# Kernel optimization log

Measured on AMD Instinct MI355X. Metric: run time of the kernel, lower is better.

Reference implementation:

```python
import jax, jax.numpy as jnp
import numpy as np

N = 20000      # nodes
E = 320000     # edges (avg degree 16)
F_IN = 32      # raw node feature dim
D = 128        # GNN_EMBEDDING_DIM = out_channels per head
HEADS = 4
RNN_H = 128    # RNN_HIDDEN_DIM
NEG_SLOPE = 0.2


def setup_inputs() -> dict:
    key = jax.random.key(0)
    ks = jax.random.split(key, 16)
    s = 0.05
    return {
        "node_features": jax.random.normal(ks[0], (N, F_IN), jnp.float32),
        "hidden_state": jax.random.normal(ks[1], (1, RNN_H), jnp.float32),
        "W_enc": jax.random.normal(ks[2], (F_IN, D), jnp.float32) * s,
        "b_enc": jax.random.normal(ks[3], (D,), jnp.float32) * s,
        "W_l": jax.random.normal(ks[4], (D, HEADS * D), jnp.float32) * s,
        "b_l": jax.random.normal(ks[5], (HEADS * D,), jnp.float32) * s,
        "W_r": jax.random.normal(ks[6], (D, HEADS * D), jnp.float32) * s,
        "b_r": jax.random.normal(ks[7], (HEADS * D,), jnp.float32) * s,
        "att": jax.random.normal(ks[8], (HEADS, D), jnp.float32) * s,
        "gat_bias": jax.random.normal(ks[9], (D,), jnp.float32) * s,
        "W_ih": jax.random.normal(ks[10], (3 * RNN_H, D), jnp.float32) * s,
        "W_hh": jax.random.normal(ks[11], (3 * RNN_H, RNN_H), jnp.float32) * s,
        "b_ih": jax.random.normal(ks[12], (3 * RNN_H,), jnp.float32) * s,
        "b_hh": jax.random.normal(ks[13], (3 * RNN_H,), jnp.float32) * s,
        "edge_index": jax.random.randint(ks[14], (2, E), 0, N, jnp.int32),
    }


def reference(node_features, hidden_state, W_enc, b_enc, W_l, b_l, W_r, b_r,
              att, gat_bias, W_ih, W_hh, b_ih, b_hh, edge_index):
    n = node_features.shape[0]
    # node encoder + ReLU
    h = jax.nn.relu(node_features @ W_enc + b_enc)                 # [N, D]

    # GATv2Conv (heads=4, concat=False), add_self_loops=True, eval (no dropout)
    loop = jnp.arange(n, dtype=edge_index.dtype)
    src = jnp.concatenate([edge_index[0], loop])                   # source j
    dst = jnp.concatenate([edge_index[1], loop])                   # target i

    xl = (h @ W_l + b_l).reshape(n, HEADS, D)                      # source proj
    xr = (h @ W_r + b_r).reshape(n, HEADS, D)                      # target proj

    e = jax.nn.leaky_relu(xl[src] + xr[dst], NEG_SLOPE)            # [Et, H, C]
    logits = jnp.einsum('ehc,hc->eh', e, att)                      # [Et, H]

    # segment softmax over incoming edges of each target node
    m = jax.ops.segment_max(logits, dst, num_segments=n)           # [N, H]
    m = jnp.where(jnp.isfinite(m), m, 0.0)
    p = jnp.exp(logits - m[dst])
    denom = jax.ops.segment_sum(p, dst, num_segments=n)
    alpha = p / jnp.maximum(denom[dst], 1e-16)                     # [Et, H]

    out = jax.ops.segment_sum(xl[src] * alpha[..., None], dst, num_segments=n)
    gat = out.mean(axis=1) + gat_bias                              # [N, D]

    # agent node 0 -> GRUCell (torch gate order: r, z, n)
    x = gat[0:1]                                                   # [1, D]
    gi = x @ W_ih.T + b_ih
    gh = hidden_state @ W_hh.T + b_hh
    i_r, i_z, i_n = jnp.split(gi, 3, axis=-1)
    h_r, h_z, h_n = jnp.split(gh, 3, axis=-1)
    r = jax.nn.sigmoid(i_r + h_r)
    z = jax.nn.sigmoid(i_z + h_z)
    ng = jnp.tanh(i_n + r * h_n)
    return (1.0 - z) * ng + z * hidden_state                       # [1, RNN_H]
```

## Files before the change

kernel.cpp:

```cpp
#include <hip/hip_runtime.h>


#define NW   32
#define NS   96
#define NBLK (NW + NS)
#define SLOTS 8
#define CAP  40
#define FLAGMAGIC 0x5A5A0000u

#define WEo  0
#define WLo  4096
#define WRo  6144
#define HSo  8192
#define XLo  0
#define LGLo 20480
#define ALPo 21760
#define WIo  21920
#define WHo  23456
#define BUFSZ 24992

#define A_H0  0
#define A_XR  128
#define A_XRP 144
#define A_HP  208
#define A_GH  336
#define A_GIB 348
#define A_GAT 360
#define A_LGP 488
#define A_NF0 528
#define A_BI  560
#define A_BHH 572
#define AUXSZ 584

struct KP {
    const int* ei; int E;
    const float *nf, *W_enc, *b_enc, *W_l, *b_l, *W_r, *b_r, *att, *gat_bias,
                *hprev, *W_ih, *W_hh, *b_ih, *b_hh;
    unsigned *scnt;
    unsigned *xlflag;
    float *hsslot;
    float *lgpart;
    float *xlpub;
    float *out;
};

__device__ __forceinline__ unsigned pollFlag(unsigned* p) {
    for (long it = 0; it < 20000000L; ++it) {
        unsigned v = atomicOr(p, 0u);
        if ((v & 0xFFFF0000u) == FLAGMAGIC) return v & 0xFFFFu;
    }
    return 0u;
}

__device__ __forceinline__ float sigm(float x) { return 1.f / (1.f + expf(-x)); }

__global__ __launch_bounds__(256) void k_all(KP p)
{
    __shared__ __align__(16) float buf[BUFSZ];
    __shared__ __align__(16) float aux[AUXSZ];
    __shared__ int iaux[208];
    const int t = threadIdx.x, b = blockIdx.x;

    if (b >= NW) {
        int s = b - NW;
        if (t == 0) iaux[0] = 0;
        __syncthreads();
        if ((p.E & 3) == 0) {
            int nv = p.E >> 2;
            int per = (nv + NS - 1) / NS;
            int lo = s * per, hi = min(lo + per, nv);
            const int4* d4 = (const int4*)(p.ei + p.E);
            for (int base = lo; base < hi; base += 1024) {
                int4 v[4];
                #pragma unroll
                for (int k = 0; k < 4; ++k) {
                    int i = base + t + k * 256;
                    v[k] = (i < hi) ? d4[i] : make_int4(1, 1, 1, 1);
                }
                #pragma unroll
                for (int k = 0; k < 4; ++k) {
                    int i = base + t + k * 256;
                    if (v[k].x == 0 || v[k].y == 0 || v[k].z == 0 || v[k].w == 0) {
                        #pragma unroll
                        for (int c = 0; c < 4; ++c) {
                            if ((&v[k].x)[c] == 0) {
                                int q = atomicAdd(&iaux[0], 1);
                                if (q < SLOTS) iaux[8 + q] = p.ei[4 * (long)i + c];
                            }
                        }
                    }
                }
            }
        } else {
            int per = (p.E + NS - 1) / NS;
            long lo = (long)s * per, hi = lo + per; if (hi > p.E) hi = p.E;
            for (long i = lo + t; i < hi; i += 256) {
                if (p.ei[p.E + i] == 0) {
                    int q = atomicAdd(&iaux[0], 1);
                    if (q < SLOTS) iaux[8 + q] = p.ei[i];
                }
            }
        }
        for (int idx = t; idx < 1024; idx += 256)
            ((float4*)(buf + WEo))[idx] = ((const float4*)p.W_enc)[idx];
        float bev = (t < 128) ? p.b_enc[t] : 0.f;
        __syncthreads();
        int myc = min(iaux[0], SLOTS);
        if (myc > 0) {
            for (int idx = t; idx < myc * 8; idx += 256) {
                int e = idx >> 3, f4 = idx & 7;
                ((float4*)aux)[e * 8 + f4] =
                    *(const float4*)(p.nf + (long)iaux[8 + e] * 32 + f4 * 4);
            }
            __syncthreads();
            for (int e = 0; e < myc; ++e) {
                if (t < 128) {
                    const float* x = aux + e * 32;
                    float a0 = 0, a1 = 0, a2 = 0, a3 = 0;
                    #pragma unroll
                    for (int k = 0; k < 32; k += 4) {
                        a0 += x[k]     * buf[WEo + k * 128 + t];
                        a1 += x[k + 1] * buf[WEo + (k + 1) * 128 + t];
                        a2 += x[k + 2] * buf[WEo + (k + 2) * 128 + t];
                        a3 += x[k + 3] * buf[WEo + (k + 3) * 128 + t];
                    }
                    p.hsslot[(long)(s * SLOTS + e) * 128 + t] =
                        fmaxf(a0 + a1 + a2 + a3 + bev, 0.f);
                }
            }
        }
        __syncthreads();
        __threadfence();
        if (t == 0) atomicExch(&p.scnt[s * 16], FLAGMAGIC | (unsigned)myc);
        return;
    }

    const int l4 = t & 15, g16 = t >> 4;
    const int j = b * 16 + l4;

    float blv = p.b_l[j], atv = p.att[j];
    float bev = (t < 128) ? p.b_enc[t] : 0.f;
    float brv = (t < 16) ? p.b_r[b * 16 + t] : 0.f;
    if (t < 128) { aux[A_HP + t] = p.hprev[t]; aux[A_GAT + t] = p.gat_bias[t]; }
    if (t >= 128 && t < 140) {
        int rr = t - 128;
        int grow = (rr >> 2) * 128 + b * 4 + (rr & 3);
        aux[A_BI + rr] = p.b_ih[grow];
        aux[A_BHH + rr] = p.b_hh[grow];
    }
    if (t >= 192 && t < 224) aux[A_NF0 + (t - 192)] = p.nf[t - 192];

    for (int idx = t; idx < 1024; idx += 256)
        ((float4*)(buf + WEo))[idx] = ((const float4*)p.W_enc)[idx];
    for (int idx = t; idx < 512; idx += 256) {
        int row = idx >> 2, f4 = idx & 3;
        ((float4*)(buf + WLo))[idx] = *(const float4*)(p.W_l + (long)row * 512 + b * 16 + f4 * 4);
        ((float4*)(buf + WRo))[idx] = *(const float4*)(p.W_r + (long)row * 512 + b * 16 + f4 * 4);
    }
    for (int idx = t; idx < 384; idx += 256) {
        int rr = idx >> 5, f4 = idx & 31;
        int grow = (rr >> 2) * 128 + b * 4 + (rr & 3);
        ((float4*)(buf + WIo))[idx] = *(const float4*)(p.W_ih + (long)grow * 128 + f4 * 4);
        ((float4*)(buf + WHo))[idx] = *(const float4*)(p.W_hh + (long)grow * 128 + f4 * 4);
    }
    __syncthreads();

    if (t < 128) {
        float a0 = 0, a1 = 0, a2 = 0, a3 = 0;
        #pragma unroll
        for (int k = 0; k < 32; k += 4) {
            a0 += aux[A_NF0 + k]     * buf[WEo + k * 128 + t];
            a1 += aux[A_NF0 + k + 1] * buf[WEo + (k + 1) * 128 + t];
            a2 += aux[A_NF0 + k + 2] * buf[WEo + (k + 2) * 128 + t];
            a3 += aux[A_NF0 + k + 3] * buf[WEo + (k + 3) * 128 + t];
        }
        aux[A_H0 + t] = fmaxf(a0 + a1 + a2 + a3 + bev, 0.f);
    }
    __syncthreads();
    if (t < 64) {
        int col = t & 15, ch = t >> 4;
        float s = 0.f;
        #pragma unroll 8
        for (int cc = 0; cc < 32; ++cc) {
            int c = ch * 32 + cc;
            s += aux[A_H0 + c] * buf[WRo + c * 16 + col];
        }
        aux[A_XRP + t] = s;
    }
    __syncthreads();
    if (t < 16) aux[A_XR + t] = aux[A_XRP + t] + aux[A_XRP + 16 + t]
                              + aux[A_XRP + 32 + t] + aux[A_XRP + 48 + t] + brv;
    {
        int w = t >> 6, l = t & 63;
        #pragma unroll
        for (int i = 0; i < 3; ++i) {
            int rr = w * 3 + i;
            float2 wv = ((const float2*)&buf[WHo + rr * 128])[l];
            float pp = wv.x * aux[A_HP + 2 * l] + wv.y * aux[A_HP + 2 * l + 1];
            #pragma unroll
            for (int off = 32; off; off >>= 1) pp += __shfl_down(pp, off);
            if (l == 0) aux[A_GH + rr] = pp + aux[A_BHH + rr];
        }
    }
    {
        int w = t >> 6, l = t & 63;
        #pragma unroll
        for (int i = 0; i < 3; ++i) {
            int rr = w * 3 + i;
            float2 wv = ((const float2*)&buf[WIo + rr * 128])[l];
            float pp = wv.x * aux[A_GAT + 2 * l] + wv.y * aux[A_GAT + 2 * l + 1];
            #pragma unroll
            for (int off = 32; off; off >>= 1) pp += __shfl_down(pp, off);
            if (l == 0) aux[A_GIB + rr] = pp + aux[A_BI + rr];
        }
    }

    if (t < NS) iaux[t] = (int)pollFlag(&p.scnt[t * 16]);
    __syncthreads();
    __threadfence();
    if (t < 64) {
        int s0 = 2 * t, s1 = 2 * t + 1;
        int c0 = (s0 < NS) ? iaux[s0] : 0;
        int c1 = (s1 < NS) ? iaux[s1] : 0;
        int sum = c0 + c1, pre = sum;
        #pragma unroll
        for (int off = 1; off < 64; off <<= 1) {
            int v = __shfl_up(pre, off);
            if (t >= off) pre += v;
        }
        int base = pre - sum;
        for (int u = 0; u < c0; ++u) { if (base < CAP - 1) iaux[104 + base] = s0 * SLOTS + u; ++base; }
        for (int u = 0; u < c1; ++u) { if (base < CAP - 1) iaux[104 + base] = s1 * SLOTS + u; ++base; }
        if (t == 63) iaux[100] = min(pre, CAP - 1);
    }
    __syncthreads();
    int Mc = iaux[100];
    int Mt = Mc + 1;

    for (int idx = t; idx < Mc * 32; idx += 256) {
        int e = idx >> 5, f4 = idx & 31;
        ((float4*)(buf + HSo))[e * 32 + f4] =
            *(const float4*)(p.hsslot + (long)iaux[104 + e] * 128 + f4 * 4);
    }
    if (t < 128) buf[HSo + Mc * 128 + t] = aux[A_H0 + t];
    __syncthreads();

    int ne = 0, el[3] = {0, 0, 0};
    for (int e = g16; e < Mt; e += 16) el[ne++] = e;
    float acc[3] = {0, 0, 0};
    #pragma unroll 4
    for (int c = 0; c < 128; c += 4) {
        float w0 = buf[WLo + c * 16 + l4],       w1 = buf[WLo + (c + 1) * 16 + l4];
        float w2 = buf[WLo + (c + 2) * 16 + l4], w3 = buf[WLo + (c + 3) * 16 + l4];
        #pragma unroll
        for (int k = 0; k < 3; ++k) {
            if (k < ne) {
                float4 h4 = *(const float4*)&buf[HSo + el[k] * 128 + c];
                acc[k] += h4.x * w0 + h4.y * w1 + h4.z * w2 + h4.w * w3;
            }
        }
    }
    {
        float xrj = aux[A_XR + l4];
        #pragma unroll
        for (int k = 0; k < 3; ++k) {
            if (k < ne) {
                int e = el[k];
                float xv = acc[k] + blv;
                p.xlpub[(long)e * 512 + j] = xv;
                float v = xv + xrj;
                v = (v > 0.f) ? v : 0.2f * v;
                float pp = v * atv;
                #pragma unroll
                for (int off = 8; off; off >>= 1) pp += __shfl_down(pp, off, 16);
                if (l4 == 0) aux[A_LGP + e] = pp;
            }
        }
    }
    __syncthreads();
    if (t < Mt) p.lgpart[b * CAP + t] = aux[A_LGP + t];
    __syncthreads();
    __threadfence();
    if (t == 0) atomicExch(&p.xlflag[b * 16], FLAGMAGIC | 1u);

    if (t < NW) pollFlag(&p.xlflag[t * 16]);
    __syncthreads();
    __threadfence();
    for (int idx = t; idx < Mt * 128; idx += 256)
        ((float4*)(buf + XLo))[idx] = ((const float4*)p.xlpub)[idx];
    for (int idx = t; idx < 320; idx += 256)
        ((float4*)(buf + LGLo))[idx] = ((const float4*)p.lgpart)[idx];
    __syncthreads();
    if (t < 4) {
        int h = t;
        float m = -1e30f;
        for (int e = 0; e < Mt; ++e) {
            float lv = 0.f;
            #pragma unroll
            for (int q = 0; q < 8; ++q) lv += buf[LGLo + (8 * h + q) * CAP + e];
            buf[ALPo + e * 4 + h] = lv;
            m = fmaxf(m, lv);
        }
        float d = 0.f;
        for (int e = 0; e < Mt; ++e) d += expf(buf[ALPo + e * 4 + h] - m);
        float inv = 1.f / fmaxf(d, 1e-16f);
        for (int e = 0; e < Mt; ++e)
            buf[ALPo + e * 4 + h] = expf(buf[ALPo + e * 4 + h] - m) * inv;
    }
    __syncthreads();
    if (t < 128) {
        float s0 = 0, s1 = 0, s2 = 0, s3 = 0;
        for (int e = 0; e < Mt; ++e) {
            const float* al = &buf[ALPo + e * 4];
            const float* xr = &buf[XLo + e * 512];
            s0 += al[0] * xr[t];
            s1 += al[1] * xr[128 + t];
            s2 += al[2] * xr[256 + t];
            s3 += al[3] * xr[384 + t];
        }
        aux[A_GAT + t] = 0.25f * (s0 + s1 + s2 + s3);
    }
    __syncthreads();
    {
        int w = t >> 6, l = t & 63;
        #pragma unroll
        for (int i = 0; i < 3; ++i) {
            int rr = w * 3 + i;
            float2 wv = ((const float2*)&buf[WIo + rr * 128])[l];
            float pp = wv.x * aux[A_GAT + 2 * l] + wv.y * aux[A_GAT + 2 * l + 1];
            #pragma unroll
            for (int off = 32; off; off >>= 1) pp += __shfl_down(pp, off);
            if (l == 0) aux[A_XRP + rr] = pp + aux[A_GIB + rr];
        }
    }
    __syncthreads();
    if (t < 4) {
        int c = b * 4 + t;
        float r = sigm(aux[A_XRP + t]     + aux[A_GH + t]);
        float z = sigm(aux[A_XRP + 4 + t] + aux[A_GH + 4 + t]);
        float n = tanhf(aux[A_XRP + 8 + t] + r * aux[A_GH + 8 + t]);
        p.out[c] = (1.f - z) * n + z * aux[A_HP + c];
    }
}

extern "C" void kernel_launch(void* const* d_in, const int* in_sizes, int n_in,
                              void* d_out, int out_size, void* d_ws, size_t ws_size,
                              hipStream_t stream) {
    KP kp;
    kp.nf       = (const float*)d_in[0];
    kp.hprev    = (const float*)d_in[1];
    kp.W_enc    = (const float*)d_in[2];
    kp.b_enc    = (const float*)d_in[3];
    kp.W_l      = (const float*)d_in[4];
    kp.b_l      = (const float*)d_in[5];
    kp.W_r      = (const float*)d_in[6];
    kp.b_r      = (const float*)d_in[7];
    kp.att      = (const float*)d_in[8];
    kp.gat_bias = (const float*)d_in[9];
    kp.W_ih     = (const float*)d_in[10];
    kp.W_hh     = (const float*)d_in[11];
    kp.b_ih     = (const float*)d_in[12];
    kp.b_hh     = (const float*)d_in[13];
    kp.ei       = (const int*)d_in[14];
    kp.E = in_sizes[14] / 2;

    char* ws = (char*)d_ws;
    kp.scnt   = (unsigned*)(ws + 0);
    kp.xlflag = (unsigned*)(ws + 6144);
    kp.hsslot = (float*)(ws + 8192);
    kp.lgpart = (float*)(ws + 401408);
    kp.xlpub  = (float*)(ws + 406528);
    kp.out    = (float*)d_out;

    k_all<<<NBLK, 256, 0, stream>>>(kp);
}
```

Measured before the change: 109.1 us.

## Split persistent flag-synchronized kernel into three sequential launches

Replaces the single cooperative kernel, which used global atomic flags and spin-polling between scanner and worker blocks, with three separate launches: edge scan/encode, per-column projection/logits, and final softmax/aggregation/GRU. Kernel boundaries now provide the ordering, removing the spin-waits and fences. The node-0 encoding moves into scan block 0 and the W_hh GRU part moves into the final kernel. In exchange it pays two extra launch overheads and loses the overlap of weight loading with the scan.

```diff
diff --git a/kernel.cpp b/kernel.cpp
--- a/kernel.cpp
+++ b/kernel.cpp
@@ -3,180 +3,130 @@
 
 #define NW   32
 #define NS   96
-#define NBLK (NW + NS)
 #define SLOTS 8
 #define CAP  40
-#define FLAGMAGIC 0x5A5A0000u
-
-#define WEo  0
-#define WLo  4096
-#define WRo  6144
-#define HSo  8192
-#define XLo  0
-#define LGLo 20480
-#define ALPo 21760
-#define WIo  21920
-#define WHo  23456
-#define BUFSZ 24992
-
-#define A_H0  0
-#define A_XR  128
-#define A_XRP 144
-#define A_HP  208
-#define A_GH  336
-#define A_GIB 348
-#define A_GAT 360
-#define A_LGP 488
-#define A_NF0 528
-#define A_BI  560
-#define A_BHH 572
-#define AUXSZ 584
 
 struct KP {
     const int* ei; int E;
     const float *nf, *W_enc, *b_enc, *W_l, *b_l, *W_r, *b_r, *att, *gat_bias,
                 *hprev, *W_ih, *W_hh, *b_ih, *b_hh;
     unsigned *scnt;
-    unsigned *xlflag;
     float *hsslot;
     float *lgpart;
     float *xlpub;
     float *out;
 };
 
-__device__ __forceinline__ unsigned pollFlag(unsigned* p) {
-    for (long it = 0; it < 20000000L; ++it) {
-        unsigned v = atomicOr(p, 0u);
-        if ((v & 0xFFFF0000u) == FLAGMAGIC) return v & 0xFFFFu;
-    }
-    return 0u;
-}
-
 __device__ __forceinline__ float sigm(float x) { return 1.f / (1.f + expf(-x)); }
 
-__global__ __launch_bounds__(256) void k_all(KP p)
+__global__ __launch_bounds__(256) void k_scan(KP p)
 {
-    __shared__ __align__(16) float buf[BUFSZ];
-    __shared__ __align__(16) float aux[AUXSZ];
-    __shared__ int iaux[208];
-    const int t = threadIdx.x, b = blockIdx.x;
-
-    if (b >= NW) {
-        int s = b - NW;
-        if (t == 0) iaux[0] = 0;
-        __syncthreads();
-        if ((p.E & 3) == 0) {
-            int nv = p.E >> 2;
-            int per = (nv + NS - 1) / NS;
-            int lo = s * per, hi = min(lo + per, nv);
-            const int4* d4 = (const int4*)(p.ei + p.E);
-            for (int base = lo; base < hi; base += 1024) {
-                int4 v[4];
-                #pragma unroll
-                for (int k = 0; k < 4; ++k) {
-                    int i = base + t + k * 256;
-                    v[k] = (i < hi) ? d4[i] : make_int4(1, 1, 1, 1);
-                }
-                #pragma unroll
-                for (int k = 0; k < 4; ++k) {
-                    int i = base + t + k * 256;
-                    if (v[k].x == 0 || v[k].y == 0 || v[k].z == 0 || v[k].w == 0) {
-                        #pragma unroll
-                        for (int c = 0; c < 4; ++c) {
-                            if ((&v[k].x)[c] == 0) {
-                                int q = atomicAdd(&iaux[0], 1);
-                                if (q < SLOTS) iaux[8 + q] = p.ei[4 * (long)i + c];
-                            }
+    __shared__ __align__(16) float wenc[4096];
+    __shared__ __align__(16) float nfr[(SLOTS + 1) * 32];
+    __shared__ int iaux[16];
+    const int t = threadIdx.x, s = blockIdx.x;
+    if (t == 0) iaux[0] = 0;
+    __syncthreads();
+    if ((p.E & 3) == 0) {
+        int nv = p.E >> 2;
+        int per = (nv + NS - 1) / NS;
+        int lo = s * per, hi = min(lo + per, nv);
+        const int4* d4 = (const int4*)(p.ei + p.E);
+        for (int base = lo; base < hi; base += 1024) {
+            int4 v[4];
+            #pragma unroll
+            for (int k = 0; k < 4; ++k) {
+                int i = base + t + k * 256;
+                v[k] = (i < hi) ? d4[i] : make_int4(1, 1, 1, 1);
+            }
+            #pragma unroll
+            for (int k = 0; k < 4; ++k) {
+                int i = base + t + k * 256;
+                if (v[k].x == 0 || v[k].y == 0 || v[k].z == 0 || v[k].w == 0) {
+                    #pragma unroll
+                    for (int c = 0; c < 4; ++c) {
+                        if ((&v[k].x)[c] == 0) {
+                            int q = atomicAdd(&iaux[0], 1);
+                            if (q < SLOTS) iaux[8 + q] = p.ei[4 * (long)i + c];
                         }
                     }
                 }
             }
-        } else {
-            int per = (p.E + NS - 1) / NS;
-            long lo = (long)s * per, hi = lo + per; if (hi > p.E) hi = p.E;
-            for (long i = lo + t; i < hi; i += 256) {
-                if (p.ei[p.E + i] == 0) {
-                    int q = atomicAdd(&iaux[0], 1);
-                    if (q < SLOTS) iaux[8 + q] = p.ei[i];
+        }
+    } else {
+        int per = (p.E + NS - 1) / NS;
+        long lo = (long)s * per, hi = lo + per; if (hi > p.E) hi = p.E;
+        for (long i = lo + t; i < hi; i += 256) {
+            if (p.ei[p.E + i] == 0) {
+                int q = atomicAdd(&iaux[0], 1);
+                if (q < SLOTS) iaux[8 + q] = p.ei[i];
+            }
+        }
+    }
+    for (int idx = t; idx < 1024; idx += 256)
+        ((float4*)wenc)[idx] = ((const float4*)p.W_enc)[idx];
+    float bev = (t < 128) ? p.b_enc[t] : 0.f;
+    __syncthreads();
+    int myc = min(iaux[0], SLOTS);
+    int M2 = myc + (s == 0 ? 1 : 0);
+    if (M2 > 0) {
+        for (int idx = t; idx < M2 * 8; idx += 256) {
+            int e = idx >> 3, f4 = idx & 7;
+            long src = (e < myc) ? (long)iaux[8 + e] : 0L;
+            ((float4*)nfr)[e * 8 + f4] =
+                *(const float4*)(p.nf + src * 32 + f4 * 4);
+        }
+        __syncthreads();
+        for (int e = 0; e < M2; ++e) {
+            if (t < 128) {
+                const float* x = nfr + e * 32;
+                float a0 = 0, a1 = 0, a2 = 0, a3 = 0;
+                #pragma unroll
+                for (int k = 0; k < 32; k += 4) {
+                    a0 += x[k]     * wenc[k * 128 + t];
+                    a1 += x[k + 1] * wenc[(k + 1) * 128 + t];
+                    a2 += x[k + 2] * wenc[(k + 2) * 128 + t];
+                    a3 += x[k + 3] * wenc[(k + 3) * 128 + t];
                 }
-            }
-        }
-        for (int idx = t; idx < 1024; idx += 256)
-            ((float4*)(buf + WEo))[idx] = ((const float4*)p.W_enc)[idx];
-        float bev = (t < 128) ? p.b_enc[t] : 0.f;
-        __syncthreads();
-        int myc = min(iaux[0], SLOTS);
-        if (myc > 0) {
-            for (int idx = t; idx < myc * 8; idx += 256) {
-                int e = idx >> 3, f4 = idx & 7;
-                ((float4*)aux)[e * 8 + f4] =
-                    *(const float4*)(p.nf + (long)iaux[8 + e] * 32 + f4 * 4);
-            }
-            __syncthreads();
-            for (int e = 0; e < myc; ++e) {
-                if (t < 128) {
-                    const float* x = aux + e * 32;
-                    float a0 = 0, a1 = 0, a2 = 0, a3 = 0;
-                    #pragma unroll
-                    for (int k = 0; k < 32; k += 4) {
-                        a0 += x[k]     * buf[WEo + k * 128 + t];
-                        a1 += x[k + 1] * buf[WEo + (k + 1) * 128 + t];
-                        a2 += x[k + 2] * buf[WEo + (k + 2) * 128 + t];
-                        a3 += x[k + 3] * buf[WEo + (k + 3) * 128 + t];
-                    }
-                    p.hsslot[(long)(s * SLOTS + e) * 128 + t] =
-                        fmaxf(a0 + a1 + a2 + a3 + bev, 0.f);
-                }
-            }
-        }
-        __syncthreads();
-        __threadfence();
-        if (t == 0) atomicExch(&p.scnt[s * 16], FLAGMAGIC | (unsigned)myc);
-        return;
-    }
-
+                long row = (e < myc) ? (long)(s * SLOTS + e) : (long)(NS * SLOTS);
+                p.hsslot[row * 128 + t] = fmaxf(a0 + a1 + a2 + a3 + bev, 0.f);
+            }
+        }
+    }
+    if (t == 0) p.scnt[s * 16] = (unsigned)myc;
+}
+
+#define WLo  0
+#define WRo  2048
+#define HSo  4096
+#define G_BUF (4096 + CAP * 128)
+
+#define A_H0  0
+#define A_XR  128
+#define A_XRP 144
+#define A_LGP 208
+#define G_AUX 248
+
+__global__ __launch_bounds__(256) void k_gemm(KP p)
+{
+    __shared__ __align__(16) float buf[G_BUF];
+    __shared__ __align__(16) float aux[G_AUX];
+    __shared__ int iaux[208];
+    const int t = threadIdx.x, b = blockIdx.x;
     const int l4 = t & 15, g16 = t >> 4;
     const int j = b * 16 + l4;
 
     float blv = p.b_l[j], atv = p.att[j];
-    float bev = (t < 128) ? p.b_enc[t] : 0.f;
     float brv = (t < 16) ? p.b_r[b * 16 + t] : 0.f;
-    if (t < 128) { aux[A_HP + t] = p.hprev[t]; aux[A_GAT + t] = p.gat_bias[t]; }
-    if (t >= 128 && t < 140) {
-        int rr = t - 128;
-        int grow = (rr >> 2) * 128 + b * 4 + (rr & 3);
-        aux[A_BI + rr] = p.b_ih[grow];
-        aux[A_BHH + rr] = p.b_hh[grow];
-    }
-    if (t >= 192 && t < 224) aux[A_NF0 + (t - 192)] = p.nf[t - 192];
-
-    for (int idx = t; idx < 1024; idx += 256)
-        ((float4*)(buf + WEo))[idx] = ((const float4*)p.W_enc)[idx];
+    if (t < 128) aux[A_H0 + t] = p.hsslot[(long)(NS * SLOTS) * 128 + t];
+    if (t < 96) iaux[t] = (int)p.scnt[t * 16];
     for (int idx = t; idx < 512; idx += 256) {
         int row = idx >> 2, f4 = idx & 3;
         ((float4*)(buf + WLo))[idx] = *(const float4*)(p.W_l + (long)row * 512 + b * 16 + f4 * 4);
         ((float4*)(buf + WRo))[idx] = *(const float4*)(p.W_r + (long)row * 512 + b * 16 + f4 * 4);
     }
-    for (int idx = t; idx < 384; idx += 256) {
-        int rr = idx >> 5, f4 = idx & 31;
-        int grow = (rr >> 2) * 128 + b * 4 + (rr & 3);
-        ((float4*)(buf + WIo))[idx] = *(const float4*)(p.W_ih + (long)grow * 128 + f4 * 4);
-        ((float4*)(buf + WHo))[idx] = *(const float4*)(p.W_hh + (long)grow * 128 + f4 * 4);
-    }
-    __syncthreads();
-
-    if (t < 128) {
-        float a0 = 0, a1 = 0, a2 = 0, a3 = 0;
-        #pragma unroll
-        for (int k = 0; k < 32; k += 4) {
-            a0 += aux[A_NF0 + k]     * buf[WEo + k * 128 + t];
-            a1 += aux[A_NF0 + k + 1] * buf[WEo + (k + 1) * 128 + t];
-            a2 += aux[A_NF0 + k + 2] * buf[WEo + (k + 2) * 128 + t];
-            a3 += aux[A_NF0 + k + 3] * buf[WEo + (k + 3) * 128 + t];
-        }
-        aux[A_H0 + t] = fmaxf(a0 + a1 + a2 + a3 + bev, 0.f);
-    }
-    __syncthreads();
+    __syncthreads();
+
     if (t < 64) {
         int col = t & 15, ch = t >> 4;
         float s = 0.f;
@@ -190,34 +140,6 @@
     __syncthreads();
     if (t < 16) aux[A_XR + t] = aux[A_XRP + t] + aux[A_XRP + 16 + t]
                               + aux[A_XRP + 32 + t] + aux[A_XRP + 48 + t] + brv;
-    {
-        int w = t >> 6, l = t & 63;
-        #pragma unroll
-        for (int i = 0; i < 3; ++i) {
-            int rr = w * 3 + i;
-            float2 wv = ((const float2*)&buf[WHo + rr * 128])[l];
-            float pp = wv.x * aux[A_HP + 2 * l] + wv.y * aux[A_HP + 2 * l + 1];
-            #pragma unroll
-            for (int off = 32; off; off >>= 1) pp += __shfl_down(pp, off);
-            if (l == 0) aux[A_GH + rr] = pp + aux[A_BHH + rr];
-        }
-    }
-    {
-        int w = t >> 6, l = t & 63;
-        #pragma unroll
-        for (int i = 0; i < 3; ++i) {
-            int rr = w * 3 + i;
-            float2 wv = ((const float2*)&buf[WIo + rr * 128])[l];
-            float pp = wv.x * aux[A_GAT + 2 * l] + wv.y * aux[A_GAT + 2 * l + 1];
-            #pragma unroll
-            for (int off = 32; off; off >>= 1) pp += __shfl_down(pp, off);
-            if (l == 0) aux[A_GIB + rr] = pp + aux[A_BI + rr];
-        }
-    }
-
-    if (t < NS) iaux[t] = (int)pollFlag(&p.scnt[t * 16]);
-    __syncthreads();
-    __threadfence();
     if (t < 64) {
         int s0 = 2 * t, s1 = 2 * t + 1;
         int c0 = (s0 < NS) ? iaux[s0] : 0;
@@ -279,13 +201,82 @@
     }
     __syncthreads();
     if (t < Mt) p.lgpart[b * CAP + t] = aux[A_LGP + t];
-    __syncthreads();
-    __threadfence();
-    if (t == 0) atomicExch(&p.xlflag[b * 16], FLAGMAGIC | 1u);
-
-    if (t < NW) pollFlag(&p.xlflag[t * 16]);
-    __syncthreads();
-    __threadfence();
+}
+
+#define XLo  0
+#define LGLo 20480
+#define ALPo 21760
+#define WIo  21920
+#define WHo  23456
+#define F_BUF 24992
+
+#define B_HP  0
+#define B_GH  128
+#define B_GIB 140
+#define B_GAT 152
+#define B_BI  280
+#define B_BHH 292
+#define B_GI  304
+#define F_AUX 316
+
+__global__ __launch_bounds__(256) void k_final(KP p)
+{
+    __shared__ __align__(16) float buf[F_BUF];
+    __shared__ __align__(16) float aux[F_AUX];
+    __shared__ int iaux[104];
+    const int t = threadIdx.x, b = blockIdx.x;
+
+    if (t < 128) { aux[B_HP + t] = p.hprev[t]; aux[B_GAT + t] = p.gat_bias[t]; }
+    if (t >= 128 && t < 140) {
+        int rr = t - 128;
+        int grow = (rr >> 2) * 128 + b * 4 + (rr & 3);
+        aux[B_BI + rr] = p.b_ih[grow];
+        aux[B_BHH + rr] = p.b_hh[grow];
+    }
+    if (t < 96) iaux[t] = (int)p.scnt[t * 16];
+    for (int idx = t; idx < 384; idx += 256) {
+        int rr = idx >> 5, f4 = idx & 31;
+        int grow = (rr >> 2) * 128 + b * 4 + (rr & 3);
+        ((float4*)(buf + WIo))[idx] = *(const float4*)(p.W_ih + (long)grow * 128 + f4 * 4);
+        ((float4*)(buf + WHo))[idx] = *(const float4*)(p.W_hh + (long)grow * 128 + f4 * 4);
+    }
+    __syncthreads();
+    {
+        int w = t >> 6, l = t & 63;
+        #pragma unroll
+        for (int i = 0; i < 3; ++i) {
+            int rr = w * 3 + i;
+            float2 wv = ((const float2*)&buf[WHo + rr * 128])[l];
+            float pp = wv.x * aux[B_HP + 2 * l] + wv.y * aux[B_HP + 2 * l + 1];
+            #pragma unroll
+            for (int off = 32; off; off >>= 1) pp += __shfl_down(pp, off);
+            if (l == 0) aux[B_GH + rr] = pp + aux[B_BHH + rr];
+        }
+    }
+    {
+        int w = t >> 6, l = t & 63;
+        #pragma unroll
+        for (int i = 0; i < 3; ++i) {
+            int rr = w * 3 + i;
+            float2 wv = ((const float2*)&buf[WIo + rr * 128])[l];
+            float pp = wv.x * aux[B_GAT + 2 * l] + wv.y * aux[B_GAT + 2 * l + 1];
+            #pragma unroll
+            for (int off = 32; off; off >>= 1) pp += __shfl_down(pp, off);
+            if (l == 0) aux[B_GIB + rr] = pp + aux[B_BI + rr];
+        }
+    }
+    if (t < 64) {
+        int s0 = 2 * t, s1 = 2 * t + 1;
+        int c0 = (s0 < NS) ? min(iaux[s0], SLOTS) : 0;
+        int c1 = (s1 < NS) ? min(iaux[s1], SLOTS) : 0;
+        int sum = c0 + c1;
+        #pragma unroll
+        for (int off = 32; off; off >>= 1) sum += __shfl_down(sum, off);
+        if (t == 0) iaux[100] = min(sum, CAP - 1);
+    }
+    __syncthreads();
+    int Mt = iaux[100] + 1;
+
     for (int idx = t; idx < Mt * 128; idx += 256)
         ((float4*)(buf + XLo))[idx] = ((const float4*)p.xlpub)[idx];
     for (int idx = t; idx < 320; idx += 256)
@@ -318,7 +309,7 @@
             s2 += al[2] * xr[256 + t];
             s3 += al[3] * xr[384 + t];
         }
-        aux[A_GAT + t] = 0.25f * (s0 + s1 + s2 + s3);
+        aux[B_GAT + t] = 0.25f * (s0 + s1 + s2 + s3);
     }
     __syncthreads();
     {
@@ -327,19 +318,19 @@
         for (int i = 0; i < 3; ++i) {
             int rr = w * 3 + i;
             float2 wv = ((const float2*)&buf[WIo + rr * 128])[l];
-            float pp = wv.x * aux[A_GAT + 2 * l] + wv.y * aux[A_GAT + 2 * l + 1];
+            float pp = wv.x * aux[B_GAT + 2 * l] + wv.y * aux[B_GAT + 2 * l + 1];
             #pragma unroll
             for (int off = 32; off; off >>= 1) pp += __shfl_down(pp, off);
-            if (l == 0) aux[A_XRP + rr] = pp + aux[A_GIB + rr];
+            if (l == 0) aux[B_GI + rr] = pp + aux[B_GIB + rr];
         }
     }
     __syncthreads();
     if (t < 4) {
         int c = b * 4 + t;
-        float r = sigm(aux[A_XRP + t]     + aux[A_GH + t]);
-        float z = sigm(aux[A_XRP + 4 + t] + aux[A_GH + 4 + t]);
-        float n = tanhf(aux[A_XRP + 8 + t] + r * aux[A_GH + 8 + t]);
-        p.out[c] = (1.f - z) * n + z * aux[A_HP + c];
+        float r = sigm(aux[B_GI + t]     + aux[B_GH + t]);
+        float z = sigm(aux[B_GI + 4 + t] + aux[B_GH + 4 + t]);
+        float n = tanhf(aux[B_GI + 8 + t] + r * aux[B_GH + 8 + t]);
+        p.out[c] = (1.f - z) * n + z * aux[B_HP + c];
     }
 }
 
@@ -366,11 +357,12 @@
 
     char* ws = (char*)d_ws;
     kp.scnt   = (unsigned*)(ws + 0);
-    kp.xlflag = (unsigned*)(ws + 6144);
     kp.hsslot = (float*)(ws + 8192);
-    kp.lgpart = (float*)(ws + 401408);
-    kp.xlpub  = (float*)(ws + 406528);
+    kp.lgpart = (float*)(ws + 401920);
+    kp.xlpub  = (float*)(ws + 407040);
     kp.out    = (float*)d_out;
 
-    k_all<<<NBLK, 256, 0, stream>>>(kp);
+    k_scan <<<NS, 256, 0, stream>>>(kp);
+    k_gemm <<<NW, 256, 0, stream>>>(kp);
+    k_final<<<NW, 256, 0, stream>>>(kp);
 }
```

Result: faster. 104.9 us (-3.9%).

## Collapse worker blocks into one consumer block, scanners compute xl projections

Applied to the files above, without the earlier changes.

Replaces the 32 cooperating worker blocks with a single consumer block and drops the second inter-block flag barrier. Scanner blocks now compute the W_l projection of their found source nodes and publish xl rows directly. The one consumer block does all of xr, the GRU gate products, the attention softmax and the aggregation serially. This removes a grid-wide handshake and its polling latency, but the single block now streams all of W_l/W_r/W_ih/W_hh by itself, adding serial work.

```diff
diff --git a/kernel.cpp b/kernel.cpp
--- a/kernel.cpp
+++ b/kernel.cpp
@@ -1,45 +1,43 @@
 #include <hip/hip_runtime.h>
 
 
-#define NW   32
-#define NS   96
-#define NBLK (NW + NS)
+#define NSB  96
+#define NBLK 97
 #define SLOTS 8
 #define CAP  40
 #define FLAGMAGIC 0x5A5A0000u
 
+#define XLo  0
+#define SLC  20480
+#define XR0  28672
+#define ATTo 29184
+#define PRT  29696
+#define ALP  30976
+#define BUFSZ 31136
+
 #define WEo  0
-#define WLo  4096
-#define WRo  6144
-#define HSo  8192
-#define XLo  0
-#define LGLo 20480
-#define ALPo 21760
-#define WIo  21920
-#define WHo  23456
-#define BUFSZ 24992
-
-#define A_H0  0
-#define A_XR  128
-#define A_XRP 144
-#define A_HP  208
-#define A_GH  336
-#define A_GIB 348
-#define A_GAT 360
-#define A_LGP 488
-#define A_NF0 528
-#define A_BI  560
-#define A_BHH 572
-#define AUXSZ 584
+#define WLS  4096
+#define HSL  12288
+
+#define A_H0   0
+#define A_HP   128
+#define A_GB   256
+#define A_NF0  384
+#define A_GH   416
+#define A_GIB  800
+#define A_GI   1184
+#define A_BI   1568
+#define A_BH   1952
+#define A_GAT  2336
+#define A_SM   2464
+#define A_T64  2472
+#define AUXSZ  2536
 
 struct KP {
     const int* ei; int E;
     const float *nf, *W_enc, *b_enc, *W_l, *b_l, *W_r, *b_r, *att, *gat_bias,
                 *hprev, *W_ih, *W_hh, *b_ih, *b_hh;
     unsigned *scnt;
-    unsigned *xlflag;
-    float *hsslot;
-    float *lgpart;
     float *xlpub;
     float *out;
 };
@@ -61,13 +59,13 @@
     __shared__ int iaux[208];
     const int t = threadIdx.x, b = blockIdx.x;
 
-    if (b >= NW) {
-        int s = b - NW;
+    if (b < NSB) {
+        const int s = b;
         if (t == 0) iaux[0] = 0;
         __syncthreads();
         if ((p.E & 3) == 0) {
             int nv = p.E >> 2;
-            int per = (nv + NS - 1) / NS;
+            int per = (nv + NSB - 1) / NSB;
             int lo = s * per, hi = min(lo + per, nv);
             const int4* d4 = (const int4*)(p.ei + p.E);
             for (int base = lo; base < hi; base += 1024) {
@@ -92,7 +90,7 @@
                 }
             }
         } else {
-            int per = (p.E + NS - 1) / NS;
+            int per = (p.E + NSB - 1) / NSB;
             long lo = (long)s * per, hi = lo + per; if (hi > p.E) hi = p.E;
             for (long i = lo + t; i < hi; i += 256) {
                 if (p.ei[p.E + i] == 0) {
@@ -124,8 +122,34 @@
                         a2 += x[k + 2] * buf[WEo + (k + 2) * 128 + t];
                         a3 += x[k + 3] * buf[WEo + (k + 3) * 128 + t];
                     }
-                    p.hsslot[(long)(s * SLOTS + e) * 128 + t] =
-                        fmaxf(a0 + a1 + a2 + a3 + bev, 0.f);
+                    buf[HSL + e * 128 + t] = fmaxf(a0 + a1 + a2 + a3 + bev, 0.f);
+                }
+            }
+            const int l4 = t & 15, g16 = t >> 4;
+            for (int sb = 0; sb < 32; sb += 4) {
+                __syncthreads();
+                for (int idx = t; idx < 2048; idx += 256) {
+                    int u = idx >> 9, r2 = idx & 511;
+                    int row = r2 >> 2, f4 = r2 & 3;
+                    ((float4*)(buf + WLS + u * 2048))[r2] =
+                        *(const float4*)(p.W_l + (long)row * 512 + (sb + u) * 16 + f4 * 4);
+                }
+                __syncthreads();
+                if (g16 < myc) {
+                    #pragma unroll
+                    for (int u = 0; u < 4; ++u) {
+                        const float* wl = buf + WLS + u * 2048;
+                        float acc = 0.f;
+                        #pragma unroll 4
+                        for (int c = 0; c < 128; c += 4) {
+                            float w0 = wl[c * 16 + l4],       w1 = wl[(c + 1) * 16 + l4];
+                            float w2 = wl[(c + 2) * 16 + l4], w3 = wl[(c + 3) * 16 + l4];
+                            float4 h4 = *(const float4*)&buf[HSL + g16 * 128 + c];
+                            acc += h4.x * w0 + h4.y * w1 + h4.z * w2 + h4.w * w3;
+                        }
+                        p.xlpub[(long)(s * SLOTS + g16) * 512 + (sb + u) * 16 + l4] =
+                            acc + p.b_l[(sb + u) * 16 + l4];
+                    }
                 }
             }
         }
@@ -135,93 +159,121 @@
         return;
     }
 
-    const int l4 = t & 15, g16 = t >> 4;
-    const int j = b * 16 + l4;
-
-    float blv = p.b_l[j], atv = p.att[j];
+    if (t < 128) { aux[A_HP + t] = p.hprev[t]; aux[A_GB + t] = p.gat_bias[t]; }
+    if (t < 32) aux[A_NF0 + t] = p.nf[t];
+    for (int idx = t; idx < 384; idx += 256) {
+        aux[A_BI + idx] = p.b_ih[idx];
+        aux[A_BH + idx] = p.b_hh[idx];
+    }
+    for (int idx = t; idx < 512; idx += 256) buf[ATTo + idx] = p.att[idx];
+    for (int idx = t; idx < 1024; idx += 256)
+        ((float4*)(buf + SLC))[idx] = ((const float4*)p.W_enc)[idx];
     float bev = (t < 128) ? p.b_enc[t] : 0.f;
-    float brv = (t < 16) ? p.b_r[b * 16 + t] : 0.f;
-    if (t < 128) { aux[A_HP + t] = p.hprev[t]; aux[A_GAT + t] = p.gat_bias[t]; }
-    if (t >= 128 && t < 140) {
-        int rr = t - 128;
-        int grow = (rr >> 2) * 128 + b * 4 + (rr & 3);
-        aux[A_BI + rr] = p.b_ih[grow];
-        aux[A_BHH + rr] = p.b_hh[grow];
-    }
-    if (t >= 192 && t < 224) aux[A_NF0 + (t - 192)] = p.nf[t - 192];
-
-    for (int idx = t; idx < 1024; idx += 256)
-        ((float4*)(buf + WEo))[idx] = ((const float4*)p.W_enc)[idx];
-    for (int idx = t; idx < 512; idx += 256) {
-        int row = idx >> 2, f4 = idx & 3;
-        ((float4*)(buf + WLo))[idx] = *(const float4*)(p.W_l + (long)row * 512 + b * 16 + f4 * 4);
-        ((float4*)(buf + WRo))[idx] = *(const float4*)(p.W_r + (long)row * 512 + b * 16 + f4 * 4);
-    }
-    for (int idx = t; idx < 384; idx += 256) {
-        int rr = idx >> 5, f4 = idx & 31;
-        int grow = (rr >> 2) * 128 + b * 4 + (rr & 3);
-        ((float4*)(buf + WIo))[idx] = *(const float4*)(p.W_ih + (long)grow * 128 + f4 * 4);
-        ((float4*)(buf + WHo))[idx] = *(const float4*)(p.W_hh + (long)grow * 128 + f4 * 4);
-    }
-    __syncthreads();
-
+    __syncthreads();
     if (t < 128) {
+        const float* x = aux + A_NF0;
         float a0 = 0, a1 = 0, a2 = 0, a3 = 0;
         #pragma unroll
         for (int k = 0; k < 32; k += 4) {
-            a0 += aux[A_NF0 + k]     * buf[WEo + k * 128 + t];
-            a1 += aux[A_NF0 + k + 1] * buf[WEo + (k + 1) * 128 + t];
-            a2 += aux[A_NF0 + k + 2] * buf[WEo + (k + 2) * 128 + t];
-            a3 += aux[A_NF0 + k + 3] * buf[WEo + (k + 3) * 128 + t];
+            a0 += x[k]     * buf[SLC + k * 128 + t];
+            a1 += x[k + 1] * buf[SLC + (k + 1) * 128 + t];
+            a2 += x[k + 2] * buf[SLC + (k + 2) * 128 + t];
+            a3 += x[k + 3] * buf[SLC + (k + 3) * 128 + t];
         }
         aux[A_H0 + t] = fmaxf(a0 + a1 + a2 + a3 + bev, 0.f);
     }
-    __syncthreads();
-    if (t < 64) {
-        int col = t & 15, ch = t >> 4;
-        float s = 0.f;
-        #pragma unroll 8
-        for (int cc = 0; cc < 32; ++cc) {
-            int c = ch * 32 + cc;
-            s += aux[A_H0 + c] * buf[WRo + c * 16 + col];
-        }
-        aux[A_XRP + t] = s;
-    }
-    __syncthreads();
-    if (t < 16) aux[A_XR + t] = aux[A_XRP + t] + aux[A_XRP + 16 + t]
-                              + aux[A_XRP + 32 + t] + aux[A_XRP + 48 + t] + brv;
-    {
-        int w = t >> 6, l = t & 63;
+
+    for (int bb = 0; bb < 32; bb += 2) {
+        __syncthreads();
+        for (int idx = t; idx < 768; idx += 256) {
+            int u = (idx < 384) ? 0 : 1, r2 = idx - u * 384;
+            int rr = r2 >> 5, f4 = r2 & 31;
+            int grow = (rr >> 2) * 128 + (bb + u) * 4 + (rr & 3);
+            ((float4*)(buf + SLC + u * 3072))[r2]        = *(const float4*)(p.W_ih + (long)grow * 128 + f4 * 4);
+            ((float4*)(buf + SLC + u * 3072 + 1536))[r2] = *(const float4*)(p.W_hh + (long)grow * 128 + f4 * 4);
+        }
+        __syncthreads();
         #pragma unroll
-        for (int i = 0; i < 3; ++i) {
-            int rr = w * 3 + i;
-            float2 wv = ((const float2*)&buf[WHo + rr * 128])[l];
-            float pp = wv.x * aux[A_HP + 2 * l] + wv.y * aux[A_HP + 2 * l + 1];
+        for (int u = 0; u < 2; ++u) {
+            int bw = bb + u;
+            int w = t >> 6, l = t & 63;
             #pragma unroll
-            for (int off = 32; off; off >>= 1) pp += __shfl_down(pp, off);
-            if (l == 0) aux[A_GH + rr] = pp + aux[A_BHH + rr];
-        }
-    }
-    {
-        int w = t >> 6, l = t & 63;
+            for (int i = 0; i < 3; ++i) {
+                int rr = w * 3 + i;
+                int grow = (rr >> 2) * 128 + bw * 4 + (rr & 3);
+                float2 wv = ((const float2*)&buf[SLC + u * 3072 + 1536 + rr * 128])[l];
+                float pp = wv.x * aux[A_HP + 2 * l] + wv.y * aux[A_HP + 2 * l + 1];
+                #pragma unroll
+                for (int off = 32; off; off >>= 1) pp += __shfl_down(pp, off);
+                if (l == 0) aux[A_GH + bw * 12 + rr] = pp + aux[A_BH + grow];
+            }
+            #pragma unroll
+            for (int i = 0; i < 3; ++i) {
+                int rr = w * 3 + i;
+                int grow = (rr >> 2) * 128 + bw * 4 + (rr & 3);
+                float2 wv = ((const float2*)&buf[SLC + u * 3072 + rr * 128])[l];
+                float pp = wv.x * aux[A_GB + 2 * l] + wv.y * aux[A_GB + 2 * l + 1];
+                #pragma unroll
+                for (int off = 32; off; off >>= 1) pp += __shfl_down(pp, off);
+                if (l == 0) aux[A_GIB + bw * 12 + rr] = pp + aux[A_BI + grow];
+            }
+        }
+    }
+
+    for (int sb = 0; sb < 32; sb += 2) {
+        __syncthreads();
+        for (int idx = t; idx < 2048; idx += 256) {
+            int u = idx >> 10, r2 = idx & 1023;
+            int m = r2 >> 9, r3 = r2 & 511;
+            int row = r3 >> 2, f4 = r3 & 3;
+            const float* src = m ? p.W_r : p.W_l;
+            ((float4*)(buf + SLC + u * 4096 + m * 2048))[r3] =
+                *(const float4*)(src + (long)row * 512 + (sb + u) * 16 + f4 * 4);
+        }
+        __syncthreads();
         #pragma unroll
-        for (int i = 0; i < 3; ++i) {
-            int rr = w * 3 + i;
-            float2 wv = ((const float2*)&buf[WIo + rr * 128])[l];
-            float pp = wv.x * aux[A_GAT + 2 * l] + wv.y * aux[A_GAT + 2 * l + 1];
-            #pragma unroll
-            for (int off = 32; off; off >>= 1) pp += __shfl_down(pp, off);
-            if (l == 0) aux[A_GIB + rr] = pp + aux[A_BI + rr];
-        }
-    }
-
-    if (t < NS) iaux[t] = (int)pollFlag(&p.scnt[t * 16]);
+        for (int u = 0; u < 2; ++u) {
+            int s2 = sb + u;
+            const float* wl = buf + SLC + u * 4096;
+            const float* wr = wl + 2048;
+            if (t < 64) {
+                int col = t & 15, ch = t >> 4;
+                float sum = 0.f;
+                #pragma unroll 8
+                for (int cc = 0; cc < 32; ++cc) {
+                    int c = ch * 32 + cc;
+                    sum += aux[A_H0 + c] * wr[c * 16 + col];
+                }
+                aux[A_T64 + t] = sum;
+            } else if (t < 80) {
+                int l4b = t - 64;
+                float acc = 0.f;
+                #pragma unroll 4
+                for (int c = 0; c < 128; c += 4) {
+                    float w0 = wl[c * 16 + l4b],       w1 = wl[(c + 1) * 16 + l4b];
+                    float w2 = wl[(c + 2) * 16 + l4b], w3 = wl[(c + 3) * 16 + l4b];
+                    float4 h4 = *(const float4*)&aux[A_H0 + c];
+                    acc += h4.x * w0 + h4.y * w1 + h4.z * w2 + h4.w * w3;
+                }
+                p.xlpub[(long)(NSB * SLOTS) * 512 + s2 * 16 + l4b] =
+                    acc + p.b_l[s2 * 16 + l4b];
+            }
+            __syncthreads();
+            if (t < 16) buf[XR0 + s2 * 16 + t] = aux[A_T64 + t] + aux[A_T64 + 16 + t]
+                                               + aux[A_T64 + 32 + t] + aux[A_T64 + 48 + t]
+                                               + p.b_r[s2 * 16 + t];
+            __syncthreads();
+        }
+    }
+
+    if (t < NSB) iaux[t] = (int)pollFlag(&p.scnt[t * 16]);
     __syncthreads();
     __threadfence();
+
     if (t < 64) {
         int s0 = 2 * t, s1 = 2 * t + 1;
-        int c0 = (s0 < NS) ? iaux[s0] : 0;
-        int c1 = (s1 < NS) ? iaux[s1] : 0;
+        int c0 = (s0 < NSB) ? iaux[s0] : 0;
+        int c1 = (s1 < NSB) ? iaux[s1] : 0;
         int sum = c0 + c1, pre = sum;
         #pragma unroll
         for (int off = 1; off < 64; off <<= 1) {
@@ -237,81 +289,66 @@
     int Mc = iaux[100];
     int Mt = Mc + 1;
 
-    for (int idx = t; idx < Mc * 32; idx += 256) {
-        int e = idx >> 5, f4 = idx & 31;
-        ((float4*)(buf + HSo))[e * 32 + f4] =
-            *(const float4*)(p.hsslot + (long)iaux[104 + e] * 128 + f4 * 4);
-    }
-    if (t < 128) buf[HSo + Mc * 128 + t] = aux[A_H0 + t];
-    __syncthreads();
-
-    int ne = 0, el[3] = {0, 0, 0};
-    for (int e = g16; e < Mt; e += 16) el[ne++] = e;
-    float acc[3] = {0, 0, 0};
-    #pragma unroll 4
-    for (int c = 0; c < 128; c += 4) {
-        float w0 = buf[WLo + c * 16 + l4],       w1 = buf[WLo + (c + 1) * 16 + l4];
-        float w2 = buf[WLo + (c + 2) * 16 + l4], w3 = buf[WLo + (c + 3) * 16 + l4];
-        #pragma unroll
-        for (int k = 0; k < 3; ++k) {
-            if (k < ne) {
-                float4 h4 = *(const float4*)&buf[HSo + el[k] * 128 + c];
-                acc[k] += h4.x * w0 + h4.y * w1 + h4.z * w2 + h4.w * w3;
-            }
-        }
-    }
+    for (int idx = t; idx < Mc * 128; idx += 256) {
+        int e = idx >> 7, f4 = idx & 127;
+        ((float4*)(buf + XLo))[e * 128 + f4] =
+            *(const float4*)(p.xlpub + (long)iaux[104 + e] * 512 + f4 * 4);
+    }
+    if (t < 128)
+        ((float4*)(buf + XLo))[Mc * 128 + t] =
+            *(const float4*)(p.xlpub + (long)(NSB * SLOTS) * 512 + t * 4);
+    __syncthreads();
+
     {
-        float xrj = aux[A_XR + l4];
-        #pragma unroll
-        for (int k = 0; k < 3; ++k) {
-            if (k < ne) {
-                int e = el[k];
-                float xv = acc[k] + blv;
-                p.xlpub[(long)e * 512 + j] = xv;
-                float v = xv + xrj;
-                v = (v > 0.f) ? v : 0.2f * v;
-                float pp = v * atv;
-                #pragma unroll
-                for (int off = 8; off; off >>= 1) pp += __shfl_down(pp, off, 16);
-                if (l4 == 0) aux[A_LGP + e] = pp;
-            }
-        }
-    }
-    __syncthreads();
-    if (t < Mt) p.lgpart[b * CAP + t] = aux[A_LGP + t];
-    __syncthreads();
-    __threadfence();
-    if (t == 0) atomicExch(&p.xlflag[b * 16], FLAGMAGIC | 1u);
-
-    if (t < NW) pollFlag(&p.xlflag[t * 16]);
-    __syncthreads();
-    __threadfence();
-    for (int idx = t; idx < Mt * 128; idx += 256)
-        ((float4*)(buf + XLo))[idx] = ((const float4*)p.xlpub)[idx];
-    for (int idx = t; idx < 320; idx += 256)
-        ((float4*)(buf + LGLo))[idx] = ((const float4*)p.lgpart)[idx];
+        const int l4 = t & 15, g16 = t >> 4;
+        for (int s2 = 0; s2 < 32; ++s2) {
+            #pragma unroll
+            for (int k = 0; k < 3; ++k) {
+                int e = g16 + 16 * k;
+                if (e < Mt) {
+                    float xv = buf[XLo + e * 512 + s2 * 16 + l4];
+                    float v = xv + buf[XR0 + s2 * 16 + l4];
+                    v = (v > 0.f) ? v : 0.2f * v;
+                    float pp = v * buf[ATTo + s2 * 16 + l4];
+                    #pragma unroll
+                    for (int off = 8; off; off >>= 1) pp += __shfl_down(pp, off, 16);
+                    if (l4 == 0) buf[PRT + e * 32 + s2] = pp;
+                }
+            }
+        }
+    }
+    __syncthreads();
+    {
+        int e = t >> 2, h = t & 3;
+        if (t < 160 && e < Mt) {
+            float lv = 0.f;
+            #pragma unroll
+            for (int q = 0; q < 8; ++q) lv += buf[PRT + e * 32 + 8 * h + q];
+            buf[ALP + e * 4 + h] = lv;
+        }
+    }
     __syncthreads();
     if (t < 4) {
         int h = t;
         float m = -1e30f;
-        for (int e = 0; e < Mt; ++e) {
-            float lv = 0.f;
-            #pragma unroll
-            for (int q = 0; q < 8; ++q) lv += buf[LGLo + (8 * h + q) * CAP + e];
-            buf[ALPo + e * 4 + h] = lv;
-            m = fmaxf(m, lv);
-        }
+        for (int e = 0; e < Mt; ++e) m = fmaxf(m, buf[ALP + e * 4 + h]);
         float d = 0.f;
-        for (int e = 0; e < Mt; ++e) d += expf(buf[ALPo + e * 4 + h] - m);
-        float inv = 1.f / fmaxf(d, 1e-16f);
-        for (int e = 0; e < Mt; ++e)
-            buf[ALPo + e * 4 + h] = expf(buf[ALPo + e * 4 + h] - m) * inv;
+        for (int e = 0; e < Mt; ++e) d += expf(buf[ALP + e * 4 + h] - m);
+        aux[A_SM + h] = m;
+        aux[A_SM + 4 + h] = 1.f / fmaxf(d, 1e-16f);
+    }
+    __syncthreads();
+    {
+        int e = t >> 2, h = t & 3;
+        if (t < 160 && e < Mt)
+            buf[ALP + e * 4 + h] =
+                expf(buf[ALP + e * 4 + h] - aux[A_SM + h]) * aux[A_SM + 4 + h];
     }
     __syncthreads();
     if (t < 128) {
         float s0 = 0, s1 = 0, s2 = 0, s3 = 0;
         for (int e = 0; e < Mt; ++e) {
-            const float* al = &buf[ALPo + e * 4];
+            const float* al = &buf[ALP + e * 4];
             const float* xr = &buf[XLo + e * 512];
             s0 += al[0] * xr[t];
             s1 += al[1] * xr[128 + t];
@@ -320,26 +357,39 @@
         }
         aux[A_GAT + t] = 0.25f * (s0 + s1 + s2 + s3);
     }
-    __syncthreads();
-    {
-        int w = t >> 6, l = t & 63;
+
+    for (int bb = 0; bb < 32; bb += 4) {
+        __syncthreads();
+        for (int idx = t; idx < 1536; idx += 256) {
+            int u = idx / 384, r2 = idx - u * 384;
+            int rr = r2 >> 5, f4 = r2 & 31;
+            int grow = (rr >> 2) * 128 + (bb + u) * 4 + (rr & 3);
+            ((float4*)(buf + SLC + u * 1536))[r2] =
+                *(const float4*)(p.W_ih + (long)grow * 128 + f4 * 4);
+        }
+        __syncthreads();
         #pragma unroll
-        for (int i = 0; i < 3; ++i) {
-            int rr = w * 3 + i;
-            float2 wv = ((const float2*)&buf[WIo + rr * 128])[l];
-            float pp = wv.x * aux[A_GAT + 2 * l] + wv.y * aux[A_GAT + 2 * l + 1];
+        for (int u = 0; u < 4; ++u) {
+            int bw = bb + u;
+            int w = t >> 6, l = t & 63;
             #pragma unroll
-            for (int off = 32; off; off >>= 1) pp += __shfl_down(pp, off);
-            if (l == 0) aux[A_XRP + rr] = pp + aux[A_GIB + rr];
-        }
-    }
-    __syncthreads();
-    if (t < 4) {
-        int c = b * 4 + t;
-        float r = sigm(aux[A_XRP + t]     + aux[A_GH + t]);
-        float z = sigm(aux[A_XRP + 4 + t] + aux[A_GH + 4 + t]);
-        float n = tanhf(aux[A_XRP + 8 + t] + r * aux[A_GH + 8 + t]);
-        p.out[c] = (1.f - z) * n + z * aux[A_HP + c];
+            for (int i = 0; i < 3; ++i) {
+                int rr = w * 3 + i;
+                float2 wv = ((const float2*)&buf[SLC + u * 1536 + rr * 128])[l];
+                float pp = wv.x * aux[A_GAT + 2 * l] + wv.y * aux[A_GAT + 2 * l + 1];
+                #pragma unroll
+                for (int off = 32; off; off >>= 1) pp += __shfl_down(pp, off);
+                if (l == 0) aux[A_GI + bw * 12 + rr] = pp + aux[A_GIB + bw * 12 + rr];
+            }
+        }
+    }
+    __syncthreads();
+    if (t < 128) {
+        int bw = t >> 2, q = t & 3;
+        float r = sigm(aux[A_GI + bw * 12 + q]     + aux[A_GH + bw * 12 + q]);
+        float z = sigm(aux[A_GI + bw * 12 + 4 + q] + aux[A_GH + bw * 12 + 4 + q]);
+        float n = tanhf(aux[A_GI + bw * 12 + 8 + q] + r * aux[A_GH + bw * 12 + 8 + q]);
+        p.out[t] = (1.f - z) * n + z * aux[A_HP + t];
     }
 }
 
@@ -366,10 +416,7 @@
 
     char* ws = (char*)d_ws;
     kp.scnt   = (unsigned*)(ws + 0);
-    kp.xlflag = (unsigned*)(ws + 6144);
-    kp.hsslot = (float*)(ws + 8192);
-    kp.lgpart = (float*)(ws + 401408);
-    kp.xlpub  = (float*)(ws + 406528);
+    kp.xlpub  = (float*)(ws + 8192);
     kp.out    = (float*)d_out;
 
     k_all<<<NBLK, 256, 0, stream>>>(kp);
```

Measured after the change: 282.8 us. 159% more time.
